# Kernel optimization log

Hardware: AMD Instinct MI355X
Metric: run time of the kernel (lower is better)

## Reference

```python
import jax, jax.numpy as jnp
import numpy as np

B, T, D, H = 4, 1024, 1024, 16
NUM_BUCKETS = 320
MAX_DIST = 800
LN_EPS = 1e-5


def _rel_bucket(T):
    # bidirectional T5-style relative position buckets
    ctx = jnp.arange(T)[:, None]
    mem = jnp.arange(T)[None, :]
    rel = mem - ctx  # (T, T)
    half = NUM_BUCKETS // 2  # 160
    bucket = (rel > 0).astype(jnp.int32) * half
    n = jnp.abs(rel)
    max_exact = half // 2  # 80
    is_small = n < max_exact
    n_f = jnp.maximum(n, 1).astype(jnp.float32)
    large = max_exact + (
        jnp.log(n_f / max_exact) / np.log(MAX_DIST / max_exact) * (half - max_exact)
    ).astype(jnp.int32)
    large = jnp.minimum(large, half - 1)
    return bucket + jnp.where(is_small, n, large)


def setup_inputs() -> dict:
    key = jax.random.key(0)
    ks = jax.random.split(key, 12)
    s = 0.02
    return {
        "x": jax.random.normal(ks[0], (B, T, D), jnp.float32),
        "ln_w": jnp.ones((D,), jnp.float32),
        "ln_b": jnp.zeros((D,), jnp.float32),
        "wq": jax.random.normal(ks[1], (D, D), jnp.float32) * s,
        "bq": jnp.zeros((D,), jnp.float32),
        "wk": jax.random.normal(ks[2], (D, D), jnp.float32) * s,
        "bk": jnp.zeros((D,), jnp.float32),
        "wv": jax.random.normal(ks[3], (D, D), jnp.float32) * s,
        "bv": jnp.zeros((D,), jnp.float32),
        "wo": jax.random.normal(ks[4], (D, D), jnp.float32) * s,
        "bo": jnp.zeros((D,), jnp.float32),
        "rel_emb": jax.random.normal(ks[5], (NUM_BUCKETS, H), jnp.float32) * s,
        "grep_w": jax.random.normal(ks[6], (8, D // H), jnp.float32) * s,
        "grep_b": jnp.zeros((8,), jnp.float32),
        "grep_a": jnp.ones((1, H, 1, 1), jnp.float32),
    }


def reference(x, ln_w, ln_b, wq, bq, wk, bk, wv, bv, wo, bo, rel_emb, grep_w, grep_b, grep_a):
    Bb, Tt, Dd = x.shape
    hd = Dd // H
    scaling = hd ** -0.5
    # pre-norm LayerNorm
    mu = jnp.mean(x, -1, keepdims=True)
    var = jnp.mean((x - mu) ** 2, -1, keepdims=True)
    h = (x - mu) / jnp.sqrt(var + LN_EPS) * ln_w + ln_b
    # projections (q pre-scaled as in fairseq/WavLM)
    q = (h @ wq.T + bq) * scaling
    k = h @ wk.T + bk
    v = h @ wv.T + bv
    q = q.reshape(Bb, Tt, H, hd).transpose(0, 2, 1, 3)  # (B,H,T,hd)
    k = k.reshape(Bb, Tt, H, hd).transpose(0, 2, 1, 3)
    v = v.reshape(Bb, Tt, H, hd).transpose(0, 2, 1, 3)
    # bucketed relative position bias: (H, T, T)
    buckets = _rel_bucket(Tt)
    pos_bias = rel_emb[buckets].transpose(2, 0, 1)
    # gru_rel_pos gating (per batch, head, query position)
    alpha = 32.0
    ql = q * (alpha / scaling)  # undo scaling, multiply by alpha
    g = jax.nn.sigmoid((ql @ grep_w.T + grep_b).reshape(Bb, H, Tt, 2, 4).sum(-1))
    gate_a, gate_b = g[..., 0:1], g[..., 1:2]  # (B,H,T,1)
    gate = gate_a * (gate_b * grep_a - 1.0) + 2.0
    # attention
    scores = jnp.einsum('bhtd,bhsd->bhts', q, k) + gate * pos_bias[None]
    attn = jax.nn.softmax(scores, axis=-1)
    out = jnp.einsum('bhts,bhsd->bhtd', attn, v).transpose(0, 2, 1, 3).reshape(Bb, Tt, Dd)
    # output projection, dropout (identity in eval), residual
    out = out @ wo.T + bo + x
    pos_bias_out = jnp.broadcast_to(pos_bias[None], (Bb, H, Tt, Tt)).reshape(Bb * H, Tt, Tt)
    return out, pos_bias_out
```

## Files before the change

### kernel.cpp

```cpp
#include <hip/hip_runtime.h>

typedef unsigned short u16;
typedef __attribute__((ext_vector_type(8))) short short8;
typedef __attribute__((ext_vector_type(4))) float floatx4;

#define MFMA16(a, b, c) __builtin_amdgcn_mfma_f32_16x16x32_bf16(a, b, c, 0, 0, 0)

__device__ __forceinline__ float bf2f(u16 u) {
  return __uint_as_float(((unsigned int)u) << 16);
}
__device__ __forceinline__ u16 f2bf(float f) {
  unsigned int u = __float_as_uint(f);
  unsigned int r = (u + 0x7fffu + ((u >> 16) & 1u)) >> 16;
  return (u16)r;
}

__global__ __launch_bounds__(256) void ln_kernel(
    const float* __restrict__ x, const float* __restrict__ w, const float* __restrict__ bb,
    u16* __restrict__ hb)
{
  int wid = threadIdx.x >> 6, lane = threadIdx.x & 63;
  int row = blockIdx.x * 4 + wid;
  const float* xr = x + row * 1024 + lane * 16;
  float xs[16];
#pragma unroll
  for (int i = 0; i < 4; i++) {
    float4 v = *(const float4*)(xr + i * 4);
    xs[i * 4 + 0] = v.x; xs[i * 4 + 1] = v.y; xs[i * 4 + 2] = v.z; xs[i * 4 + 3] = v.w;
  }
  float s = 0.f, ss = 0.f;
#pragma unroll
  for (int i = 0; i < 16; i++) { s += xs[i]; ss += xs[i] * xs[i]; }
#pragma unroll
  for (int m = 1; m < 64; m <<= 1) { s += __shfl_xor(s, m, 64); ss += __shfl_xor(ss, m, 64); }
  float mu = s * (1.0f / 1024.0f);
  float var = ss * (1.0f / 1024.0f) - mu * mu;
  float rstd = rsqrtf(var + 1e-5f);
  const float* wr = w + lane * 16;
  const float* br = bb + lane * 16;
  short8 o0, o1;
#pragma unroll
  for (int i = 0; i < 8; i++) {
    o0[i] = (short)f2bf((xs[i] - mu) * rstd * wr[i] + br[i]);
    o1[i] = (short)f2bf((xs[8 + i] - mu) * rstd * wr[8 + i] + br[8 + i]);
  }
  u16* hr = hb + row * 1024 + lane * 16;
  *(short8*)hr = o0;
  *(short8*)(hr + 8) = o1;
}

__global__ __launch_bounds__(256) void convw_kernel(
    const float* __restrict__ wq, const float* __restrict__ wk,
    const float* __restrict__ wv, const float* __restrict__ wo,
    u16* __restrict__ wb)
{
  int idx = (blockIdx.x * 256 + threadIdx.x) * 8;
  int seg = idx >> 20, off = idx & 1048575;
  const float* s = (seg == 0) ? wq : (seg == 1) ? wk : (seg == 2) ? wv : wo;
  float4 f0 = *(const float4*)(s + off);
  float4 f1 = *(const float4*)(s + off + 4);
  short8 o;
  o[0] = (short)f2bf(f0.x); o[1] = (short)f2bf(f0.y);
  o[2] = (short)f2bf(f0.z); o[3] = (short)f2bf(f0.w);
  o[4] = (short)f2bf(f1.x); o[5] = (short)f2bf(f1.y);
  o[6] = (short)f2bf(f1.z); o[7] = (short)f2bf(f1.w);
  *(short8*)&wb[idx] = o;
}

__global__ __launch_bounds__(256) void qkv_kernel(
    const u16* __restrict__ hb, const u16* __restrict__ wb,
    const float* __restrict__ bq, const float* __restrict__ bk, const float* __restrict__ bv,
    u16* __restrict__ qs, u16* __restrict__ kko, u16* __restrict__ vt)
{
  __shared__ u16 As[128 * 32];
  __shared__ u16 Bs[128 * 32];
  int tid = threadIdx.x;
  int wid = tid >> 6, lane = tid & 63;
  int wm = wid >> 1, wn = wid & 1;
  int l15 = lane & 15, quad = lane >> 4;
  int m0 = blockIdx.y * 128;
  int n0g = blockIdx.x * 128;
  int sec = n0g >> 10;
  int n0 = n0g & 1023;
  const u16* W = wb + sec * 1048576;
  const float* bias = (sec == 0) ? bq : ((sec == 1) ? bk : bv);

  floatx4 zero4 = {0.f, 0.f, 0.f, 0.f};
  floatx4 acc[4][4];
#pragma unroll
  for (int i = 0; i < 4; i++)
#pragma unroll
    for (int j = 0; j < 4; j++) acc[i][j] = zero4;

  int lr = tid >> 2;
  int lc = (tid & 3) * 8;

  for (int kt = 0; kt < 1024; kt += 32) {
    *(short8*)&As[lr * 32 + lc]        = *(const short8*)&hb[(m0 + lr) * 1024 + kt + lc];
    *(short8*)&As[(lr + 64) * 32 + lc] = *(const short8*)&hb[(m0 + lr + 64) * 1024 + kt + lc];
    *(short8*)&Bs[lr * 32 + lc]        = *(const short8*)&W[(n0 + lr) * 1024 + kt + lc];
    *(short8*)&Bs[(lr + 64) * 32 + lc] = *(const short8*)&W[(n0 + lr + 64) * 1024 + kt + lc];
    __syncthreads();
    short8 af[4], bf[4];
#pragma unroll
    for (int mi = 0; mi < 4; mi++)
      af[mi] = *(const short8*)&As[(wm * 64 + mi * 16 + l15) * 32 + quad * 8];
#pragma unroll
    for (int ni = 0; ni < 4; ni++)
      bf[ni] = *(const short8*)&Bs[(wn * 64 + ni * 16 + l15) * 32 + quad * 8];
#pragma unroll
    for (int mi = 0; mi < 4; mi++)
#pragma unroll
      for (int ni = 0; ni < 4; ni++)
        acc[mi][ni] = MFMA16(af[mi], bf[ni], acc[mi][ni]);
    __syncthreads();
  }

  int bidx = m0 >> 10;
#pragma unroll
  for (int mi = 0; mi < 4; mi++) {
#pragma unroll
    for (int ni = 0; ni < 4; ni++) {
#pragma unroll
      for (int r = 0; r < 4; r++) {
        int row = m0 + wm * 64 + mi * 16 + quad * 4 + r;
        int t = row & 1023;
        int c = n0 + wn * 64 + ni * 16 + l15;
        float val = acc[mi][ni][r] + bias[c];
        int hh = c >> 6, hp = c & 63;
        if (sec == 0) {
          val *= 0.125f;
          qs[((bidx * 16 + hh) * 1024 + t) * 64 + hp] = f2bf(val);
        } else if (sec == 1) {
          kko[((bidx * 16 + hh) * 1024 + t) * 64 + hp] = f2bf(val);
        } else {
          vt[((bidx * 16 + hh) * 64 + hp) * 1024 + t] = f2bf(val);
        }
      }
    }
  }
}

__device__ __forceinline__ int rel_bucket(int t, int s) {
  int rel = s - t;
  int bucket = (rel > 0) ? 160 : 0;
  int n = (rel < 0) ? -rel : rel;
  if (n < 80) return bucket + n;
  float a = logf((float)n / 80.0f);
  float c = a / (float)2.302585092994046;
  float v = c * 80.0f;
  int large = 80 + (int)v;
  if (large > 159) large = 159;
  return bucket + large;
}

__global__ __launch_bounds__(256) void bias0_kernel(
    const float* __restrict__ rel_emb, float* __restrict__ out1)
{
  int tid = blockIdx.x * 256 + threadIdx.x;
  int t = tid >> 7;
  int s0 = (tid & 127) * 8;
  int bkt[8];
#pragma unroll
  for (int j = 0; j < 8; j++) bkt[j] = rel_bucket(t, s0 + j) * 16;
  int base_ts = t * 1024 + s0;
#pragma unroll
  for (int hh = 0; hh < 16; hh++) {
    float4 v0, v1;
    v0.x = rel_emb[bkt[0] + hh]; v0.y = rel_emb[bkt[1] + hh];
    v0.z = rel_emb[bkt[2] + hh]; v0.w = rel_emb[bkt[3] + hh];
    v1.x = rel_emb[bkt[4] + hh]; v1.y = rel_emb[bkt[5] + hh];
    v1.z = rel_emb[bkt[6] + hh]; v1.w = rel_emb[bkt[7] + hh];
    float* p = out1 + hh * 1048576 + base_ts;
    *(float4*)p = v0;
    *(float4*)(p + 4) = v1;
  }
}

__global__ __launch_bounds__(256) void bias_copy_kernel(float* __restrict__ out1)
{
  int idx = blockIdx.x * 256 + threadIdx.x;
  float4 v = *(const float4*)&out1[idx * 4];
  *(float4*)&out1[16777216 + idx * 4] = v;
  *(float4*)&out1[33554432 + idx * 4] = v;
  *(float4*)&out1[50331648 + idx * 4] = v;
}

__global__ __launch_bounds__(256) void attn_kernel(
    const u16* __restrict__ qs, const u16* __restrict__ kko, const u16* __restrict__ vt,
    const float* __restrict__ gw, const float* __restrict__ gb, const float* __restrict__ ga,
    const float* __restrict__ bias, u16* __restrict__ ao)
{
  __shared__ __align__(16) u16 Pb[4][16 * 32];
  int wid = threadIdx.x >> 6, lane = threadIdx.x & 63;
  int l15 = lane & 15, quad = lane >> 4;
  int bh = blockIdx.x;
  int b = bh >> 4, h = bh & 15;
  int q0 = blockIdx.y * 64 + wid * 16;
  const u16* Q = qs + bh * 65536;
  const u16* K = kko + bh * 65536;
  const u16* V = vt + bh * 65536;
  const float* Bi = bias + h * 1048576;
  u16* pb = &Pb[wid][0];

  const u16* qrow = Q + (q0 + l15) * 64;
  float e[8];
#pragma unroll
  for (int i = 0; i < 8; i++) e[i] = gb[i];
  for (int j = 0; j < 64; j++) {
    float ql = bf2f(qrow[j]) * 256.0f;
#pragma unroll
    for (int i = 0; i < 8; i++) e[i] += ql * gw[i * 64 + j];
  }
  float u0 = e[0] + e[1] + e[2] + e[3];
  float u1 = e[4] + e[5] + e[6] + e[7];
  float sa = 1.0f / (1.0f + __expf(-u0));
  float sb = 1.0f / (1.0f + __expf(-u1));
  float gv = sa * (sb * ga[h] - 1.0f) + 2.0f;

  short8 qf0 = *(const short8*)&Q[(q0 + l15) * 64 + quad * 8];
  short8 qf1 = *(const short8*)&Q[(q0 + l15) * 64 + quad * 8 + 32];
  float gt[4], mrun[4], lrun[4];
#pragma unroll
  for (int r = 0; r < 4; r++) {
    gt[r] = __shfl(gv, quad * 4 + r, 64);
    mrun[r] = -1e30f;
    lrun[r] = 0.f;
  }
  floatx4 zero4 = {0.f, 0.f, 0.f, 0.f};
  floatx4 accO[4];
#pragma unroll
  for (int ni = 0; ni < 4; ni++) accO[ni] = zero4;

  for (int s0 = 0; s0 < 1024; s0 += 32) {
    floatx4 sc0 = zero4, sc1 = zero4;
    short8 kf;
    kf = *(const short8*)&K[(s0 + l15) * 64 + quad * 8];
    sc0 = MFMA16(qf0, kf, sc0);
    kf = *(const short8*)&K[(s0 + l15) * 64 + quad * 8 + 32];
    sc0 = MFMA16(qf1, kf, sc0);
    kf = *(const short8*)&K[(s0 + 16 + l15) * 64 + quad * 8];
    sc1 = MFMA16(qf0, kf, sc1);
    kf = *(const short8*)&K[(s0 + 16 + l15) * 64 + quad * 8 + 32];
    sc1 = MFMA16(qf1, kf, sc1);

#pragma unroll
    for (int r = 0; r < 4; r++) {
      int t = q0 + quad * 4 + r;
      float v0 = sc0[r] + gt[r] * Bi[t * 1024 + s0 + l15];
      float v1 = sc1[r] + gt[r] * Bi[t * 1024 + s0 + 16 + l15];
      float mt = fmaxf(v0, v1);
#pragma unroll
      for (int m = 1; m < 16; m <<= 1) mt = fmaxf(mt, __shfl_xor(mt, m, 64));
      float mnew = fmaxf(mrun[r], mt);
      float alpha = __expf(fmaxf(mrun[r] - mnew, -80.0f));
      float p0 = __expf(v0 - mnew);
      float p1 = __expf(v1 - mnew);
      float ps = p0 + p1;
#pragma unroll
      for (int m = 1; m < 16; m <<= 1) ps += __shfl_xor(ps, m, 64);
      lrun[r] = lrun[r] * alpha + ps;
      mrun[r] = mnew;
#pragma unroll
      for (int ni = 0; ni < 4; ni++) accO[ni][r] *= alpha;
      pb[(quad * 4 + r) * 32 + l15] = f2bf(p0);
      pb[(quad * 4 + r) * 32 + 16 + l15] = f2bf(p1);
    }
    __syncthreads();
    short8 pf = *(const short8*)&pb[l15 * 32 + quad * 8];
#pragma unroll
    for (int ni = 0; ni < 4; ni++) {
      short8 vf = *(const short8*)&V[(ni * 16 + l15) * 1024 + s0 + quad * 8];
      accO[ni] = MFMA16(pf, vf, accO[ni]);
    }
  }
#pragma unroll
  for (int ni = 0; ni < 4; ni++) {
#pragma unroll
    for (int r = 0; r < 4; r++) {
      int t = q0 + quad * 4 + r;
      float val = accO[ni][r] / lrun[r];
      ao[(b * 1024 + t) * 1024 + h * 64 + ni * 16 + l15] = f2bf(val);
    }
  }
}

__global__ __launch_bounds__(256) void oproj_kernel(
    const u16* __restrict__ ao, const u16* __restrict__ wob, const float* __restrict__ bo,
    const float* __restrict__ x, float* __restrict__ out)
{
  __shared__ u16 As[128 * 32];
  __shared__ u16 Bs[128 * 32];
  int tid = threadIdx.x;
  int wid = tid >> 6, lane = tid & 63;
  int wm = wid >> 1, wn = wid & 1;
  int l15 = lane & 15, quad = lane >> 4;
  int m0 = blockIdx.y * 128;
  int n0 = blockIdx.x * 128;

  floatx4 zero4 = {0.f, 0.f, 0.f, 0.f};
  floatx4 acc[4][4];
#pragma unroll
  for (int i = 0; i < 4; i++)
#pragma unroll
    for (int j = 0; j < 4; j++) acc[i][j] = zero4;

  int lr = tid >> 2;
  int lc = (tid & 3) * 8;

  for (int kt = 0; kt < 1024; kt += 32) {
    *(short8*)&As[lr * 32 + lc]        = *(const short8*)&ao[(m0 + lr) * 1024 + kt + lc];
    *(short8*)&As[(lr + 64) * 32 + lc] = *(const short8*)&ao[(m0 + lr + 64) * 1024 + kt + lc];
    *(short8*)&Bs[lr * 32 + lc]        = *(const short8*)&wob[(n0 + lr) * 1024 + kt + lc];
    *(short8*)&Bs[(lr + 64) * 32 + lc] = *(const short8*)&wob[(n0 + lr + 64) * 1024 + kt + lc];
    __syncthreads();
    short8 af[4], bf[4];
#pragma unroll
    for (int mi = 0; mi < 4; mi++)
      af[mi] = *(const short8*)&As[(wm * 64 + mi * 16 + l15) * 32 + quad * 8];
#pragma unroll
    for (int ni = 0; ni < 4; ni++)
      bf[ni] = *(const short8*)&Bs[(wn * 64 + ni * 16 + l15) * 32 + quad * 8];
#pragma unroll
    for (int mi = 0; mi < 4; mi++)
#pragma unroll
      for (int ni = 0; ni < 4; ni++)
        acc[mi][ni] = MFMA16(af[mi], bf[ni], acc[mi][ni]);
    __syncthreads();
  }

#pragma unroll
  for (int mi = 0; mi < 4; mi++) {
#pragma unroll
    for (int ni = 0; ni < 4; ni++) {
#pragma unroll
      for (int r = 0; r < 4; r++) {
        int row = m0 + wm * 64 + mi * 16 + quad * 4 + r;
        int c = n0 + wn * 64 + ni * 16 + l15;
        out[row * 1024 + c] = acc[mi][ni][r] + bo[c] + x[row * 1024 + c];
      }
    }
  }
}

extern "C" void kernel_launch(void* const* d_in, const int* in_sizes, int n_in,
                              void* d_out, int out_size, void* d_ws, size_t ws_size,
                              hipStream_t stream) {
  const float* x    = (const float*)d_in[0];
  const float* ln_w = (const float*)d_in[1];
  const float* ln_b = (const float*)d_in[2];
  const float* wq   = (const float*)d_in[3];
  const float* bq   = (const float*)d_in[4];
  const float* wk   = (const float*)d_in[5];
  const float* bk   = (const float*)d_in[6];
  const float* wv   = (const float*)d_in[7];
  const float* bv   = (const float*)d_in[8];
  const float* wo   = (const float*)d_in[9];
  const float* bo   = (const float*)d_in[10];
  const float* rel  = (const float*)d_in[11];
  const float* gw   = (const float*)d_in[12];
  const float* gb   = (const float*)d_in[13];
  const float* ga   = (const float*)d_in[14];

  float* out0  = (float*)d_out;
  float* out1f = out0 + 4194304;

  u16* hbb = (u16*)(out1f + 16777216);
  u16* wbb = (u16*)(out1f + 18874368);
  u16* qsb = (u16*)(out1f + 20971520);
  u16* kkb = (u16*)(out1f + 23068672);
  u16* vtb = (u16*)(out1f + 25165824);
  u16* aob = (u16*)(out1f + 27262976);

  ln_kernel<<<1024, 256, 0, stream>>>(x, ln_w, ln_b, hbb);
  convw_kernel<<<2048, 256, 0, stream>>>(wq, wk, wv, wo, wbb);
  qkv_kernel<<<dim3(24, 32), 256, 0, stream>>>(hbb, wbb, bq, bk, bv, qsb, kkb, vtb);
  bias0_kernel<<<512, 256, 0, stream>>>(rel, out1f);
  attn_kernel<<<dim3(64, 16), 256, 0, stream>>>(qsb, kkb, vtb, gw, gb, ga, out1f, aob);
  oproj_kernel<<<dim3(8, 32), 256, 0, stream>>>(aob, wbb + 3145728, bo, x, out0);
  bias_copy_kernel<<<16384, 256, 0, stream>>>(out1f);
}
```

Baseline: 539.2 us.

## Use workspace scratch, fuse bias replication, bf16 bias, async LDS loads, wider attn tile

Moves intermediate buffers into a separate workspace when it is large enough, so the bias kernel can write all four batch copies directly and the separate copy pass is skipped. The attention kernel now reads a bf16 copy of the position bias and processes 64 keys per iteration instead of 32. The QKV and output-projection GEMMs load tiles with global_load_lds direct-to-LDS instead of going through registers. Risks include slightly lower bias precision in the scores and a dependence on workspace size for the fused path.

Result: slower. 594.6 us (+10.3%).

```diff
diff --git a/kernel.cpp b/kernel.cpp
--- a/kernel.cpp
+++ b/kernel.cpp
@@ -13,6 +13,11 @@
   unsigned int u = __float_as_uint(f);
   unsigned int r = (u + 0x7fffu + ((u >> 16) & 1u)) >> 16;
   return (u16)r;
+}
+__device__ __forceinline__ void gl_lds16(const u16* g, u16* lds_wave_base) {
+  __builtin_amdgcn_global_load_lds(
+      (const __attribute__((address_space(1))) unsigned int*)g,
+      (__attribute__((address_space(3))) unsigned int*)lds_wave_base, 16, 0, 0);
 }
 
 __global__ __launch_bounds__(256) void ln_kernel(
@@ -94,12 +99,14 @@
 
   int lr = tid >> 2;
   int lc = (tid & 3) * 8;
+  u16* asw = As + wid * 512;
+  u16* bsw = Bs + wid * 512;
 
   for (int kt = 0; kt < 1024; kt += 32) {
-    *(short8*)&As[lr * 32 + lc]        = *(const short8*)&hb[(m0 + lr) * 1024 + kt + lc];
-    *(short8*)&As[(lr + 64) * 32 + lc] = *(const short8*)&hb[(m0 + lr + 64) * 1024 + kt + lc];
-    *(short8*)&Bs[lr * 32 + lc]        = *(const short8*)&W[(n0 + lr) * 1024 + kt + lc];
-    *(short8*)&Bs[(lr + 64) * 32 + lc] = *(const short8*)&W[(n0 + lr + 64) * 1024 + kt + lc];
+    gl_lds16(&hb[(m0 + lr) * 1024 + kt + lc],      asw);
+    gl_lds16(&hb[(m0 + lr + 64) * 1024 + kt + lc], asw + 2048);
+    gl_lds16(&W[(n0 + lr) * 1024 + kt + lc],       bsw);
+    gl_lds16(&W[(n0 + lr + 64) * 1024 + kt + lc],  bsw + 2048);
     __syncthreads();
     short8 af[4], bf[4];
 #pragma unroll
@@ -155,7 +162,8 @@
 }
 
 __global__ __launch_bounds__(256) void bias0_kernel(
-    const float* __restrict__ rel_emb, float* __restrict__ out1)
+    const float* __restrict__ rel_emb, float* __restrict__ out1,
+    u16* __restrict__ bh16, int nb4)
 {
   int tid = blockIdx.x * 256 + threadIdx.x;
   int t = tid >> 7;
@@ -174,6 +182,17 @@
     float* p = out1 + hh * 1048576 + base_ts;
     *(float4*)p = v0;
     *(float4*)(p + 4) = v1;
+    if (nb4) {
+      *(float4*)(p + 16777216) = v0; *(float4*)(p + 16777216 + 4) = v1;
+      *(float4*)(p + 33554432) = v0; *(float4*)(p + 33554432 + 4) = v1;
+      *(float4*)(p + 50331648) = v0; *(float4*)(p + 50331648 + 4) = v1;
+    }
+    short8 o;
+    o[0] = (short)f2bf(v0.x); o[1] = (short)f2bf(v0.y);
+    o[2] = (short)f2bf(v0.z); o[3] = (short)f2bf(v0.w);
+    o[4] = (short)f2bf(v1.x); o[5] = (short)f2bf(v1.y);
+    o[6] = (short)f2bf(v1.z); o[7] = (short)f2bf(v1.w);
+    *(short8*)(bh16 + hh * 1048576 + base_ts) = o;
   }
 }
 
@@ -189,9 +208,9 @@
 __global__ __launch_bounds__(256) void attn_kernel(
     const u16* __restrict__ qs, const u16* __restrict__ kko, const u16* __restrict__ vt,
     const float* __restrict__ gw, const float* __restrict__ gb, const float* __restrict__ ga,
-    const float* __restrict__ bias, u16* __restrict__ ao)
-{
-  __shared__ __align__(16) u16 Pb[4][16 * 32];
+    const u16* __restrict__ bh16, u16* __restrict__ ao)
+{
+  __shared__ __align__(16) u16 Pb[4][16 * 64];
   int wid = threadIdx.x >> 6, lane = threadIdx.x & 63;
   int l15 = lane & 15, quad = lane >> 4;
   int bh = blockIdx.x;
@@ -200,7 +219,7 @@
   const u16* Q = qs + bh * 65536;
   const u16* K = kko + bh * 65536;
   const u16* V = vt + bh * 65536;
-  const float* Bi = bias + h * 1048576;
+  const u16* Bi = bh16 + h * 1048576;
   u16* pb = &Pb[wid][0];
 
   const u16* qrow = Q + (q0 + l15) * 64;
@@ -232,46 +251,53 @@
 #pragma unroll
   for (int ni = 0; ni < 4; ni++) accO[ni] = zero4;
 
-  for (int s0 = 0; s0 < 1024; s0 += 32) {
-    floatx4 sc0 = zero4, sc1 = zero4;
+  for (int s0 = 0; s0 < 1024; s0 += 64) {
+    floatx4 sc[4];
+#pragma unroll
+    for (int j = 0; j < 4; j++) sc[j] = zero4;
     short8 kf;
-    kf = *(const short8*)&K[(s0 + l15) * 64 + quad * 8];
-    sc0 = MFMA16(qf0, kf, sc0);
-    kf = *(const short8*)&K[(s0 + l15) * 64 + quad * 8 + 32];
-    sc0 = MFMA16(qf1, kf, sc0);
-    kf = *(const short8*)&K[(s0 + 16 + l15) * 64 + quad * 8];
-    sc1 = MFMA16(qf0, kf, sc1);
-    kf = *(const short8*)&K[(s0 + 16 + l15) * 64 + quad * 8 + 32];
-    sc1 = MFMA16(qf1, kf, sc1);
+#pragma unroll
+    for (int j = 0; j < 4; j++) {
+      kf = *(const short8*)&K[(s0 + j * 16 + l15) * 64 + quad * 8];
+      sc[j] = MFMA16(qf0, kf, sc[j]);
+      kf = *(const short8*)&K[(s0 + j * 16 + l15) * 64 + quad * 8 + 32];
+      sc[j] = MFMA16(qf1, kf, sc[j]);
+    }
 
 #pragma unroll
     for (int r = 0; r < 4; r++) {
       int t = q0 + quad * 4 + r;
-      float v0 = sc0[r] + gt[r] * Bi[t * 1024 + s0 + l15];
-      float v1 = sc1[r] + gt[r] * Bi[t * 1024 + s0 + 16 + l15];
-      float mt = fmaxf(v0, v1);
+      float v[4];
+#pragma unroll
+      for (int j = 0; j < 4; j++)
+        v[j] = sc[j][r] + gt[r] * bf2f(Bi[t * 1024 + s0 + j * 16 + l15]);
+      float mt = fmaxf(fmaxf(v[0], v[1]), fmaxf(v[2], v[3]));
 #pragma unroll
       for (int m = 1; m < 16; m <<= 1) mt = fmaxf(mt, __shfl_xor(mt, m, 64));
       float mnew = fmaxf(mrun[r], mt);
       float alpha = __expf(fmaxf(mrun[r] - mnew, -80.0f));
-      float p0 = __expf(v0 - mnew);
-      float p1 = __expf(v1 - mnew);
-      float ps = p0 + p1;
+      float p[4], ps = 0.f;
+#pragma unroll
+      for (int j = 0; j < 4; j++) { p[j] = __expf(v[j] - mnew); ps += p[j]; }
 #pragma unroll
       for (int m = 1; m < 16; m <<= 1) ps += __shfl_xor(ps, m, 64);
       lrun[r] = lrun[r] * alpha + ps;
       mrun[r] = mnew;
 #pragma unroll
       for (int ni = 0; ni < 4; ni++) accO[ni][r] *= alpha;
-      pb[(quad * 4 + r) * 32 + l15] = f2bf(p0);
-      pb[(quad * 4 + r) * 32 + 16 + l15] = f2bf(p1);
+#pragma unroll
+      for (int j = 0; j < 4; j++)
+        pb[(quad * 4 + r) * 64 + j * 16 + l15] = f2bf(p[j]);
     }
     __syncthreads();
-    short8 pf = *(const short8*)&pb[l15 * 32 + quad * 8];
+    short8 pf0 = *(const short8*)&pb[l15 * 64 + quad * 8];
+    short8 pf1 = *(const short8*)&pb[l15 * 64 + 32 + quad * 8];
 #pragma unroll
     for (int ni = 0; ni < 4; ni++) {
       short8 vf = *(const short8*)&V[(ni * 16 + l15) * 1024 + s0 + quad * 8];
-      accO[ni] = MFMA16(pf, vf, accO[ni]);
+      accO[ni] = MFMA16(pf0, vf, accO[ni]);
+      vf = *(const short8*)&V[(ni * 16 + l15) * 1024 + s0 + 32 + quad * 8];
+      accO[ni] = MFMA16(pf1, vf, accO[ni]);
     }
   }
 #pragma unroll
@@ -307,12 +333,14 @@
 
   int lr = tid >> 2;
   int lc = (tid & 3) * 8;
+  u16* asw = As + wid * 512;
+  u16* bsw = Bs + wid * 512;
 
   for (int kt = 0; kt < 1024; kt += 32) {
-    *(short8*)&As[lr * 32 + lc]        = *(const short8*)&ao[(m0 + lr) * 1024 + kt + lc];
-    *(short8*)&As[(lr + 64) * 32 + lc] = *(const short8*)&ao[(m0 + lr + 64) * 1024 + kt + lc];
-    *(short8*)&Bs[lr * 32 + lc]        = *(const short8*)&wob[(n0 + lr) * 1024 + kt + lc];
-    *(short8*)&Bs[(lr + 64) * 32 + lc] = *(const short8*)&wob[(n0 + lr + 64) * 1024 + kt + lc];
+    gl_lds16(&ao[(m0 + lr) * 1024 + kt + lc],       asw);
+    gl_lds16(&ao[(m0 + lr + 64) * 1024 + kt + lc],  asw + 2048);
+    gl_lds16(&wob[(n0 + lr) * 1024 + kt + lc],      bsw);
+    gl_lds16(&wob[(n0 + lr + 64) * 1024 + kt + lc], bsw + 2048);
     __syncthreads();
     short8 af[4], bf[4];
 #pragma unroll
@@ -365,18 +393,22 @@
   float* out0  = (float*)d_out;
   float* out1f = out0 + 4194304;
 
-  u16* hbb = (u16*)(out1f + 16777216);
-  u16* wbb = (u16*)(out1f + 18874368);
-  u16* qsb = (u16*)(out1f + 20971520);
-  u16* kkb = (u16*)(out1f + 23068672);
-  u16* vtb = (u16*)(out1f + 25165824);
-  u16* aob = (u16*)(out1f + 27262976);
+  int big_ws = (ws_size >= (size_t)(96u << 20)) ? 1 : 0;
+  char* sb = big_ws ? (char*)d_ws : (char*)(out1f + 16777216);
+  u16* hbb = (u16*)(sb);
+  u16* wbb = (u16*)(sb + (8u << 20));
+  u16* qsb = (u16*)(sb + (16u << 20));
+  u16* kkb = (u16*)(sb + (24u << 20));
+  u16* vtb = (u16*)(sb + (32u << 20));
+  u16* aob = (u16*)(sb + (40u << 20));
+  u16* bhb = (u16*)(sb + (48u << 20));
 
   ln_kernel<<<1024, 256, 0, stream>>>(x, ln_w, ln_b, hbb);
   convw_kernel<<<2048, 256, 0, stream>>>(wq, wk, wv, wo, wbb);
   qkv_kernel<<<dim3(24, 32), 256, 0, stream>>>(hbb, wbb, bq, bk, bv, qsb, kkb, vtb);
-  bias0_kernel<<<512, 256, 0, stream>>>(rel, out1f);
-  attn_kernel<<<dim3(64, 16), 256, 0, stream>>>(qsb, kkb, vtb, gw, gb, ga, out1f, aob);
+  bias0_kernel<<<512, 256, 0, stream>>>(rel, out1f, bhb, big_ws);
+  attn_kernel<<<dim3(64, 16), 256, 0, stream>>>(qsb, kkb, vtb, gw, gb, ga, bhb, aob);
   oproj_kernel<<<dim3(8, 32), 256, 0, stream>>>(aob, wbb + 3145728, bo, x, out0);
-  bias_copy_kernel<<<16384, 256, 0, stream>>>(out1f);
-}
+  if (!big_ws)
+    bias_copy_kernel<<<16384, 256, 0, stream>>>(out1f);
+}
```
